# Optimization experiments

Hardware: AMD Instinct MI355X
Metric: run time of the kernel (lower is better)

The kernel has to match this reference:

```python
import jax, jax.numpy as jnp
import numpy as np

B = 256          # batch
MID = 16384      # mid_siz
OUT = 16384      # out_siz
C = 16           # channel_siz
NLVL = 8         # nlvl (== klvl here since floor(log2(OUT/2))=13 >= 8)
MIDF = MID >> NLVL   # mid_filter_siz = 64
OUTF = OUT >> NLVL   # out_filter_siz = 64
NB = 1 << NLVL       # 256 leaf branches
STD = 0.5


def setup_inputs() -> dict:
    key = jax.random.key(0)
    ks = jax.random.split(key, 6)
    in_data = jax.random.normal(ks[0], (B, MID, 2), jnp.float32)
    # learned parameters (buildRand: normal(0, 0.5) filters, zero biases)
    mid_dense = jax.random.normal(ks[1], (1, MID, 2), jnp.float32) * STD
    in_filter = jax.random.normal(ks[2], (MIDF, 1, C), jnp.float32) * STD   # conv1d [width,in,out]
    in_bias = jnp.zeros((C,), jnp.float32)
    # level lvl (1..NLVL) uses filters[lvl-1, :2**lvl]; padded to NB branches
    filters = jax.random.normal(ks[3], (NLVL, NB, 2, C, C), jnp.float32) * STD
    biases = jnp.zeros((NLVL, NB, C), jnp.float32)
    fea_dense = jax.random.normal(ks[4], (NB, C, OUTF), jnp.float32) * STD
    return dict(in_data=in_data, mid_dense=mid_dense, in_filter=in_filter,
                in_bias=in_bias, filters=filters, biases=biases, fea_dense=fea_dense)


def reference(in_data, mid_dense, in_filter, in_bias, filters, biases, fea_dense):
    # elementwise modulation then split real/imag channels: (B, 2, MID)
    x = jnp.moveaxis(in_data * mid_dense, -1, 1)
    # level-0 conv1d: kernel MIDF, stride MIDF//2 -> overlapping half-windows.
    # Split signal into half-width chunks h; window t = [h[t], h[t+1]].
    half = MIDF // 2
    h = x.reshape(B, 2, MID // half, half)                 # (B,2,512,32)
    W1 = in_filter[:half, 0, :]                            # (32,C)
    W2 = in_filter[half:, 0, :]
    s = jnp.einsum('bisw,wc->bisc', h[:, :, :-1], W1) \
        + jnp.einsum('bisw,wc->bisc', h[:, :, 1:], W2)
    s = jax.nn.relu(s + in_bias)                           # (B,2,2^(n+1)-1,C)
    state = s[:, :, None]                                  # (B,2,nb=1,L,C)
    # butterfly tree: each level doubles branches; conv kernel=2, stride=2, VALID
    for lvl in range(1, NLVL + 1):
        nb = 1 << lvl
        p = jnp.repeat(state, 2, axis=2)                   # child itk <- parent itk//2
        L = p.shape[3]                                     # odd: 2^(n+1-lvl+1)-1
        xw = p[:, :, :, :L - 1, :].reshape(B, 2, nb, (L - 1) // 2, 2, C)
        W = filters[lvl - 1, :nb]                          # (nb,2,C,C)
        bb = biases[lvl - 1, :nb]                          # (nb,C)
        state = jax.nn.relu(
            jnp.einsum('bintkc,nkcd->bintd', xw, W) + bb[None, None, :, None, :])
    feat = state[:, :, :, 0, :]                            # (B,2,NB,C): L==1 at last level
    outp = jnp.einsum('binc,ncf->binf', feat, fea_dense)   # per-branch dense projection
    R = outp[:, 0].reshape(B, OUT // 2, 2)
    I = outp[:, 1].reshape(B, OUT // 2, 2)
    out_data = ((R[:, :, 0] - I[:, :, 1]) / MID).reshape(B, OUT // 2, 1)
    return out_data, R[:, :, 1]
```

## Files before the change

kernel.cpp:

```cpp
#include <hip/hip_runtime.h>
#include <hip/hip_bf16.h>


#define OUT_HALF 2097152

typedef __attribute__((ext_vector_type(4))) float f32x4;
typedef __attribute__((ext_vector_type(8))) short s16x8;

__device__ __forceinline__ uint fsw(uint a) {
    return a ^ ((((a >> 6) ^ (a >> 8)) & 3u) << 4);
}
__device__ __forceinline__ ushort bfr(float f) {
    __hip_bfloat16 h = __float2bfloat16(f);
    union { __hip_bfloat16 h; ushort u; } cv; cv.h = h; return cv.u;
}
__device__ __forceinline__ uint pk(float a, float b) {
    return (uint)bfr(a) | ((uint)bfr(b) << 16);
}

__device__ __forceinline__ void tree_level(
    char* smb, const int lane, const int wave,
    uint AOff, uint NOff, int lgR, int lgNP, int nTiles,
    uint WOff, int wnb, uint LBOff, int bnb)
{
    const int m  = lane & 15;
    const int kg = lane >> 4;
    const int lgTPP = lgR - 4;
    for (int at = wave; at < nTiles; at += 4) {
        const int p  = at >> lgTPP;
        const int tc = at & ((1 << lgTPP) - 1);
        const int np = p & ((1 << lgNP) - 1);
        const int ii = p >> lgNP;
        s16x8 af = *(const s16x8*)(smb + AOff + (p << (lgR + 6)) +
                                   fsw((uint)((tc * 16 + m) * 64 + kg * 16)));
#pragma unroll
        for (int sib = 0; sib < 2; sib++) {
            const int nl = 2 * np + sib;
            s16x8 bf = *(const s16x8*)(smb + WOff +
                         fsw((uint)((wnb + nl) * 1024 + m * 64 + kg * 16)));
            float bv = *(const float*)(smb + LBOff + ((bnb + nl) * 16 + m) * 4);
            f32x4 acc = {bv, bv, bv, bv};
            acc = __builtin_amdgcn_mfma_f32_16x16x32_bf16(af, bf, acc, 0, 0, 0);
            const int p2 = (ii << (lgNP + 1)) + nl;
            const uint wb = NOff + (p2 << (lgR + 5));
            const int r2 = tc * 8 + kg * 2;
            *(uint*)(smb + wb + fsw((uint)(r2 * 64 + m * 4))) =
                pk(fmaxf(acc.x, 0.f), fmaxf(acc.y, 0.f));
            *(uint*)(smb + wb + fsw((uint)((r2 + 1) * 64 + m * 4))) =
                pk(fmaxf(acc.z, 0.f), fmaxf(acc.w, 0.f));
        }
    }
}

__global__ __launch_bounds__(256, 4)
void ibf_A(const float* __restrict__ in_data, const float* __restrict__ mid_dense,
           const float* __restrict__ in_filter, const float* __restrict__ in_bias,
           const float* __restrict__ filters, const float* __restrict__ biases,
           uint* __restrict__ S3)
{
    __shared__ __align__(16) char smb[29760];
    const int tid = threadIdx.x, lane = tid & 63, wave = tid >> 6;
    const int b = blockIdx.x;
    const int th = blockIdx.y >> 1;
    const int i  = blockIdx.y & 1;

    {
        const float4* inb = (const float4*)in_data + (size_t)b * 8192 + th * 2048;
        const float4* mdb = (const float4*)mid_dense + th * 2048;
        for (int mp = tid; mp < 2064; mp += 256) {
            float4 iv = inb[mp], mv = mdb[mp];
            float xa = i ? iv.y * mv.y : iv.x * mv.x;
            float xb = i ? iv.w * mv.w : iv.z * mv.z;
            *(uint*)(smb + fsw((uint)(mp * 4))) = pk(xa, xb);
        }
    }
    for (int t = tid; t < 3584; t += 256) {
        int nidx = t >> 8, r = t & 255, d = r & 15, c = r >> 4;
        int lvl = (nidx < 2) ? 1 : ((nidx < 6) ? 2 : 3);
        int n = nidx - ((1 << lvl) - 2);
        const float* src = filters + (size_t)(lvl - 1) * 131072 + n * 512 + c * 16 + d;
        *(uint*)(smb + 12416 + fsw((uint)(nidx * 1024 + d * 64 + c * 4))) = pk(src[0], src[256]);
    }
    for (int t = tid; t < 512; t += 256) {
        int c = t >> 5, w2 = t & 31;
        *(uint*)(smb + 26752 + fsw((uint)(c * 128 + w2 * 4))) =
            pk(in_filter[(2 * w2) * 16 + c], in_filter[(2 * w2 + 1) * 16 + c]);
    }
    if (tid < 240) {
        float v;
        if (tid < 224) {
            int nidx = tid >> 4;
            int lvl = (nidx < 2) ? 1 : ((nidx < 6) ? 2 : 3);
            int n = nidx - ((1 << lvl) - 2);
            v = biases[(size_t)(lvl - 1) * 4096 + n * 16 + (tid & 15)];
        } else v = in_bias[tid - 224];
        *(float*)(smb + 28800 + tid * 4) = v;
    }
    __syncthreads();

    {
        const int m = lane & 15, kg = lane >> 4;
        s16x8 b0 = *(const s16x8*)(smb + 26752 + fsw((uint)(m * 128 + kg * 16)));
        s16x8 b1 = *(const s16x8*)(smb + 26752 + fsw((uint)(m * 128 + 64 + kg * 16)));
        float bv = *(const float*)(smb + 28800 + (224 + m) * 4);
        for (int at = wave; at < 8; at += 4) {
            int tc = at;
            s16x8 a0 = *(const s16x8*)(smb + fsw((uint)((tc * 16 + m) * 64 + kg * 16)));
            s16x8 a1 = *(const s16x8*)(smb + fsw((uint)((tc * 16 + m) * 64 + 64 + kg * 16)));
            f32x4 acc = {bv, bv, bv, bv};
            acc = __builtin_amdgcn_mfma_f32_16x16x32_bf16(a0, b0, acc, 0, 0, 0);
            acc = __builtin_amdgcn_mfma_f32_16x16x32_bf16(a1, b1, acc, 0, 0, 0);
            int r2 = tc * 8 + kg * 2;
            *(uint*)(smb + 8320 + fsw((uint)(r2 * 64 + m * 4))) =
                pk(fmaxf(acc.x, 0.f), fmaxf(acc.y, 0.f));
            *(uint*)(smb + 8320 + fsw((uint)((r2 + 1) * 64 + m * 4))) =
                pk(fmaxf(acc.z, 0.f), fmaxf(acc.w, 0.f));
        }
    }
    __syncthreads();
    tree_level(smb, lane, wave, 8320, 0,    6, 0, 4, 12416, 0, 28800, 0);
    __syncthreads();
    tree_level(smb, lane, wave, 0,    8320, 5, 1, 4, 12416, 2, 28800, 2);
    __syncthreads();
    {
        const int m = lane & 15, kg = lane >> 4;
        for (int at = wave; at < 4; at += 4) {
            s16x8 af = *(const s16x8*)(smb + 8320 + (at << 10) + fsw((uint)(m * 64 + kg * 16)));
#pragma unroll
            for (int sib = 0; sib < 2; sib++) {
                int n3 = 2 * at + sib;
                s16x8 bf = *(const s16x8*)(smb + 12416 +
                             fsw((uint)((6 + n3) * 1024 + m * 64 + kg * 16)));
                float bv = *(const float*)(smb + 28800 + ((6 + n3) * 16 + m) * 4);
                f32x4 acc = {bv, bv, bv, bv};
                acc = __builtin_amdgcn_mfma_f32_16x16x32_bf16(af, bf, acc, 0, 0, 0);
                int bi = 2 * b + i;
                int t4 = th * 8 + kg * 2;
                uint idx = ((uint)(n3 * 512 + bi) * 16 + t4) * 16 + m;
                S3[idx]      = pk(fmaxf(acc.x, 0.f), fmaxf(acc.y, 0.f));
                S3[idx + 16] = pk(fmaxf(acc.z, 0.f), fmaxf(acc.w, 0.f));
            }
        }
    }
}

__global__ __launch_bounds__(256, 2)
void ibf_B(const float* __restrict__ filters, const float* __restrict__ biases,
           const uint* __restrict__ S3, char* __restrict__ S8)
{
    __shared__ __align__(16) char smb[24576];
    const int tid = threadIdx.x, lane = tid & 63, wave = tid >> 6;
    const int n3 = blockIdx.x, chunk = blockIdx.y;
    const int m = lane & 15, kg = lane >> 4;

    const float* FB1 = filters + (size_t)3 * 131072 + ((size_t)(n3 << 1)) * 512;
    const float* FB2 = filters + (size_t)4 * 131072 + ((size_t)(n3 << 2)) * 512;
    const float* FB3 = filters + (size_t)5 * 131072 + ((size_t)(n3 << 3)) * 512;
    const float* FB4 = filters + (size_t)6 * 131072 + ((size_t)(n3 << 4)) * 512;
    const float* FB5 = filters + (size_t)7 * 131072 + ((size_t)(n3 << 5)) * 512;
    const float* BB1 = biases + (size_t)3 * 4096 + (n3 << 1) * 16;
    const float* BB2 = biases + (size_t)4 * 4096 + (n3 << 2) * 16;
    const float* BB3 = biases + (size_t)5 * 4096 + (n3 << 3) * 16;
    const float* BB4 = biases + (size_t)6 * 4096 + (n3 << 4) * 16;
    const float* BB5 = biases + (size_t)7 * 4096 + (n3 << 5) * 16;

#define LDFRAG(dst, fb, nl)                                                  \
    {                                                                        \
        const float* s_ = (fb) + (nl) * 512 + m;                             \
        _Pragma("unroll")                                                    \
        for (int c4 = 0; c4 < 4; c4++) {                                     \
            int c_ = kg * 4 + c4;                                            \
            (&(dst).x)[c4] = pk(s_[c_ * 16], s_[256 + c_ * 16]);             \
        }                                                                    \
    }

    uint4 f4[2], f5[4];
    float b4[2], b5[4];
    LDFRAG(f4[0], FB1, 0); LDFRAG(f4[1], FB1, 1);
    b4[0] = BB1[m]; b4[1] = BB1[16 + m];
#pragma unroll
    for (int s = 0; s < 4; s++) { LDFRAG(f5[s], FB2, s); b5[s] = BB2[s * 16 + m]; }
    {
        const char* src = (const char*)S3 + ((size_t)n3 * 512 + chunk * 8) * 1024;
        for (int ci = tid; ci < 512; ci += 256)
            *(float4*)(smb + fsw((uint)(ci * 16))) = *(const float4*)(src + ci * 16);
    }
    __syncthreads();

    uint4 f6[4];
    float b6[4];
    {
        const int n0 = (wave >> 1) * 2;
        LDFRAG(f6[0], FB3, n0);     b6[0] = BB3[(n0) * 16 + m];
        LDFRAG(f6[1], FB3, n0 + 1); b6[1] = BB3[(n0 + 1) * 16 + m];
        LDFRAG(f6[2], FB3, n0 + 4); b6[2] = BB3[(n0 + 4) * 16 + m];
        LDFRAG(f6[3], FB3, n0 + 5); b6[3] = BB3[(n0 + 5) * 16 + m];
    }
#pragma unroll
    for (int t2 = 0; t2 < 2; t2++) {
        const int tc = wave + t2 * 4;
        s16x8 af = *(const s16x8*)(smb + fsw((uint)((tc * 16 + m) * 64 + kg * 16)));
#pragma unroll
        for (int sib = 0; sib < 2; sib++) {
            f32x4 acc = {b4[sib], b4[sib], b4[sib], b4[sib]};
            acc = __builtin_amdgcn_mfma_f32_16x16x32_bf16(af, *(const s16x8*)&f4[sib], acc, 0, 0, 0);
            const uint wb = 8192u + (uint)sib * 4096u;
            const int r2 = tc * 8 + kg * 2;
            *(uint*)(smb + wb + fsw((uint)(r2 * 64 + m * 4))) = pk(fmaxf(acc.x, 0.f), fmaxf(acc.y, 0.f));
            *(uint*)(smb + wb + fsw((uint)((r2 + 1) * 64 + m * 4))) = pk(fmaxf(acc.z, 0.f), fmaxf(acc.w, 0.f));
        }
    }
    __syncthreads();

    uint4 f7[4];
    float b7[4];
    {
        LDFRAG(f7[0], FB4, 2 * wave);     b7[0] = BB4[(2 * wave) * 16 + m];
        LDFRAG(f7[1], FB4, 2 * wave + 1); b7[1] = BB4[(2 * wave + 1) * 16 + m];
        LDFRAG(f7[2], FB4, 2 * wave + 8); b7[2] = BB4[(2 * wave + 8) * 16 + m];
        LDFRAG(f7[3], FB4, 2 * wave + 9); b7[3] = BB4[(2 * wave + 9) * 16 + m];
    }
#pragma unroll
    for (int t2 = 0; t2 < 2; t2++) {
        const int at = wave + t2 * 4;
        const int p = at >> 2, tc = at & 3;
        s16x8 af = *(const s16x8*)(smb + 8192 + p * 4096 + fsw((uint)((tc * 16 + m) * 64 + kg * 16)));
#pragma unroll
        for (int sib = 0; sib < 2; sib++) {
            const int nl = 2 * p + sib;
            f32x4 acc = {b5[nl], b5[nl], b5[nl], b5[nl]};
            acc = __builtin_amdgcn_mfma_f32_16x16x32_bf16(af, *(const s16x8*)&f5[nl], acc, 0, 0, 0);
            const uint wb = (uint)nl * 2048u;
            const int r2 = tc * 8 + kg * 2;
            *(uint*)(smb + wb + fsw((uint)(r2 * 64 + m * 4))) = pk(fmaxf(acc.x, 0.f), fmaxf(acc.y, 0.f));
            *(uint*)(smb + wb + fsw((uint)((r2 + 1) * 64 + m * 4))) = pk(fmaxf(acc.z, 0.f), fmaxf(acc.w, 0.f));
        }
    }
    __syncthreads();

    uint4 f8[8];
    float b8[8];
#pragma unroll
    for (int t4 = 0; t4 < 4; t4++) {
        const int at = wave + 4 * t4;
        LDFRAG(f8[2 * t4],     FB5, 2 * at);     b8[2 * t4]     = BB5[(2 * at) * 16 + m];
        LDFRAG(f8[2 * t4 + 1], FB5, 2 * at + 1); b8[2 * t4 + 1] = BB5[(2 * at + 1) * 16 + m];
    }
#pragma unroll
    for (int t2 = 0; t2 < 2; t2++) {
        const int at = wave + t2 * 4;
        const int p = at >> 1, tc = at & 1;
        s16x8 af = *(const s16x8*)(smb + p * 2048 + fsw((uint)((tc * 16 + m) * 64 + kg * 16)));
#pragma unroll
        for (int sib = 0; sib < 2; sib++) {
            const int nl = 2 * p + sib;
            const int fi = t2 * 2 + sib;
            f32x4 acc = {b6[fi], b6[fi], b6[fi], b6[fi]};
            acc = __builtin_amdgcn_mfma_f32_16x16x32_bf16(af, *(const s16x8*)&f6[fi], acc, 0, 0, 0);
            const uint wb = 8192u + (uint)nl * 1024u;
            const int r2 = tc * 8 + kg * 2;
            *(uint*)(smb + wb + fsw((uint)(r2 * 64 + m * 4))) = pk(fmaxf(acc.x, 0.f), fmaxf(acc.y, 0.f));
            *(uint*)(smb + wb + fsw((uint)((r2 + 1) * 64 + m * 4))) = pk(fmaxf(acc.z, 0.f), fmaxf(acc.w, 0.f));
        }
    }
    __syncthreads();

#pragma unroll
    for (int t2 = 0; t2 < 2; t2++) {
        const int p = wave + t2 * 4;
        s16x8 af = *(const s16x8*)(smb + 8192 + p * 1024 + fsw((uint)(m * 64 + kg * 16)));
#pragma unroll
        for (int sib = 0; sib < 2; sib++) {
            const int nl = 2 * p + sib;
            const int fi = t2 * 2 + sib;
            f32x4 acc = {b7[fi], b7[fi], b7[fi], b7[fi]};
            acc = __builtin_amdgcn_mfma_f32_16x16x32_bf16(af, *(const s16x8*)&f7[fi], acc, 0, 0, 0);
            const uint wb = (uint)nl * 512u;
            const int r2 = kg * 2;
            *(uint*)(smb + wb + fsw((uint)(r2 * 64 + m * 4))) = pk(fmaxf(acc.x, 0.f), fmaxf(acc.y, 0.f));
            *(uint*)(smb + wb + fsw((uint)((r2 + 1) * 64 + m * 4))) = pk(fmaxf(acc.z, 0.f), fmaxf(acc.w, 0.f));
        }
    }
    __syncthreads();

#pragma unroll
    for (int t4 = 0; t4 < 4; t4++) {
        const int at = wave + 4 * t4;
        s16x8 af = *(const s16x8*)(smb + at * 512 + fsw((uint)(m * 64 + kg * 16)));
#pragma unroll
        for (int sib = 0; sib < 2; sib++) {
            const int nl = 2 * at + sib;
            const int fi = t4 * 2 + sib;
            f32x4 acc = {b8[fi], b8[fi], b8[fi], b8[fi]};
            acc = __builtin_amdgcn_mfma_f32_16x16x32_bf16(af, *(const s16x8*)&f8[fi], acc, 0, 0, 0);
            if (kg < 2) {
                float v[4] = {fmaxf(acc.x, 0.f), fmaxf(acc.y, 0.f),
                              fmaxf(acc.z, 0.f), fmaxf(acc.w, 0.f)};
#pragma unroll
                for (int j = 0; j < 4; j++)
                    *(ushort*)(smb + 16384 + nl * 256 + (kg * 4 + j) * 32 + m * 2) = bfr(v[j]);
            }
        }
    }
    __syncthreads();
    {
        float4* dst = (float4*)(S8 + (size_t)(n3 * 64 + chunk) * 8192);
        for (int ci = tid; ci < 512; ci += 256)
            dst[ci] = *(const float4*)(smb + 16384 + ci * 16);
    }
#undef LDFRAG
}

__global__ __launch_bounds__(256, 4)
void ibf_C(const float* __restrict__ fea_dense, const char* __restrict__ S8,
           float* __restrict__ out)
{
    __shared__ ushort FEb[1024];
    const int tid = threadIdx.x, lane = tid & 63, wave = tid >> 6;
    const int n8g = blockIdx.x, q = blockIdx.y;
    const int n3 = n8g >> 5, n8l = n8g & 31;

    for (int idx = tid; idx < 1024; idx += 256) {
        int c = idx >> 6, u = idx & 63;
        FEb[u * 16 + c] = bfr(fea_dense[(size_t)n8g * 1024 + idx]);
    }
    __syncthreads();

    const int m = lane & 15, kg = lane >> 4;
    s16x8 bfrg[4];
#pragma unroll
    for (int ut = 0; ut < 4; ut++) {
        if (kg < 2) bfrg[ut] = *(const s16x8*)(FEb + (ut * 16 + m) * 16 + kg * 8);
        else        bfrg[ut] = (s16x8){0, 0, 0, 0, 0, 0, 0, 0};
    }
    for (int w = 0; w < 2; w++) {
        const int tile  = q * 8 + wave * 2 + w;
        const int birow = tile * 16 + m;
        s16x8 af = {0, 0, 0, 0, 0, 0, 0, 0};
        if (kg < 2)
            af = *(const s16x8*)(S8 + ((size_t)(n3 * 64 + (birow >> 3)) * 32 + n8l) * 256
                                 + (birow & 7) * 32 + kg * 16);
        const int b0  = (tile * 16 + kg * 4) >> 1;
        const bool odd = (m & 1);
#pragma unroll
        for (int ut = 0; ut < 4; ut++) {
            f32x4 acc = {0.f, 0.f, 0.f, 0.f};
            acc = __builtin_amdgcn_mfma_f32_16x16x32_bf16(af, bfrg[ut], acc, 0, 0, 0);
            float sy = __shfl_xor(acc.y, 1);
            float sw = __shfl_xor(acc.w, 1);
            const int g = n8g * 32 + ut * 8 + (m >> 1);
            float v0 = odd ? acc.x : (acc.x - sy) * (1.f / 16384.f);
            float v1 = odd ? acc.z : (acc.z - sw) * (1.f / 16384.f);
            size_t off = (odd ? (size_t)OUT_HALF : (size_t)0) + (size_t)g;
            out[(size_t)b0 * 8192 + off]       = v0;
            out[(size_t)(b0 + 1) * 8192 + off] = v1;
        }
    }
}

extern "C" void kernel_launch(void* const* d_in, const int* in_sizes, int n_in,
                              void* d_out, int out_size, void* d_ws, size_t ws_size,
                              hipStream_t stream) {
    const float* in_data   = (const float*)d_in[0];
    const float* mid_dense = (const float*)d_in[1];
    const float* in_filter = (const float*)d_in[2];
    const float* in_bias   = (const float*)d_in[3];
    const float* filters   = (const float*)d_in[4];
    const float* biases    = (const float*)d_in[5];
    const float* fea_dense = (const float*)d_in[6];
    float* out = (float*)d_out;
    uint* S3   = (uint*)d_ws;
    char* S8   = (char*)d_ws + (4 << 20);

    ibf_A<<<dim3(256, 4), 256, 0, stream>>>(in_data, mid_dense, in_filter, in_bias,
                                            filters, biases, S3);
    ibf_B<<<dim3(8, 64), 256, 0, stream>>>(filters, biases, S3, S8);
    ibf_C<<<dim3(256, 4), 256, 0, stream>>>(fea_dense, S8, out);
}
```

Measured before the change: 40.55 us.

## Fuse final tree stage with dense projection kernel, eliminating S8 round trip

Merges the last-stage tree kernel and the per-branch dense projection kernel into one kernel. Leaf features stay in shared memory in a swizzled, zero-padded layout and feed the projection MFMA directly, so the S8 workspace write/read and one kernel launch are gone. In exchange, each block now reloads and converts fea_dense from global memory with strided scalar loads, repeated across the 64 chunk blocks. It also raises shared memory per block, and each block does less projection work with fewer lanes active.

```diff
diff --git a/kernel.cpp b/kernel.cpp
--- a/kernel.cpp
+++ b/kernel.cpp
@@ -145,13 +145,17 @@
 }
 
 __global__ __launch_bounds__(256, 2)
-void ibf_B(const float* __restrict__ filters, const float* __restrict__ biases,
-           const uint* __restrict__ S3, char* __restrict__ S8)
+void ibf_BC(const float* __restrict__ filters, const float* __restrict__ biases,
+            const float* __restrict__ fea_dense, const uint* __restrict__ S3,
+            float* __restrict__ out)
 {
-    __shared__ __align__(16) char smb[24576];
+    __shared__ __align__(16) char smb[33536];
     const int tid = threadIdx.x, lane = tid & 63, wave = tid >> 6;
     const int n3 = blockIdx.x, chunk = blockIdx.y;
     const int m = lane & 15, kg = lane >> 4;
+
+    for (int o = tid * 16; o < 16384; o += 4096)
+        *(float4*)(smb + 16384 + o) = make_float4(0.f, 0.f, 0.f, 0.f);
 
     const float* FB1 = filters + (size_t)3 * 131072 + ((size_t)(n3 << 1)) * 512;
     const float* FB2 = filters + (size_t)4 * 131072 + ((size_t)(n3 << 2)) * 512;
@@ -297,65 +301,48 @@
                 float v[4] = {fmaxf(acc.x, 0.f), fmaxf(acc.y, 0.f),
                               fmaxf(acc.z, 0.f), fmaxf(acc.w, 0.f)};
 #pragma unroll
-                for (int j = 0; j < 4; j++)
-                    *(ushort*)(smb + 16384 + nl * 256 + (kg * 4 + j) * 32 + m * 2) = bfr(v[j]);
+                for (int j = 0; j < 4; j++) {
+                    uint o = (uint)(nl * 512 + (kg * 4 + j) * 64 + m * 2);
+                    *(ushort*)(smb + 16384 + fsw(o)) = bfr(v[j]);
+                }
             }
         }
     }
     __syncthreads();
-    {
-        float4* dst = (float4*)(S8 + (size_t)(n3 * 64 + chunk) * 8192);
-        for (int ci = tid; ci < 512; ci += 256)
-            dst[ci] = *(const float4*)(smb + 16384 + ci * 16);
+
+    for (int q = 0; q < 8; q++) {
+        int n8l = wave * 8 + q;
+        int gn8 = n3 * 32 + n8l;
+        s16x8 af = *(const s16x8*)(smb + 16384 +
+                     fsw((uint)(n8l * 512 + m * 64 + kg * 16)));
+        const float* fb = fea_dense + (size_t)gn8 * 1024;
+#pragma unroll
+        for (int ut = 0; ut < 4; ut++) {
+            s16x8 bf = {0, 0, 0, 0, 0, 0, 0, 0};
+            if (kg < 2) {
+                const float* fp = fb + kg * 512 + ut * 16 + m;
+                bf[0] = (short)bfr(fp[0]);   bf[1] = (short)bfr(fp[64]);
+                bf[2] = (short)bfr(fp[128]); bf[3] = (short)bfr(fp[192]);
+                bf[4] = (short)bfr(fp[256]); bf[5] = (short)bfr(fp[320]);
+                bf[6] = (short)bfr(fp[384]); bf[7] = (short)bfr(fp[448]);
+            }
+            f32x4 acc = {0.f, 0.f, 0.f, 0.f};
+            acc = __builtin_amdgcn_mfma_f32_16x16x32_bf16(af, bf, acc, 0, 0, 0);
+            float s0 = __shfl_xor(acc.y, 1);
+            float s2 = __shfl_xor(acc.w, 1);
+            if (kg < 2) {
+                int g = gn8 * 32 + ut * 8 + (m >> 1);
+                bool odd = (m & 1);
+                float v0 = odd ? acc.x : (acc.x - s0) * (1.f / 16384.f);
+                float v1 = odd ? acc.z : (acc.z - s2) * (1.f / 16384.f);
+                size_t off = (odd ? (size_t)OUT_HALF : (size_t)0) + (size_t)g;
+                int b0 = chunk * 4 + kg * 2;
+                out[(size_t)b0 * 8192 + off]       = v0;
+                out[(size_t)(b0 + 1) * 8192 + off] = v1;
+            }
+        }
     }
 #undef LDFRAG
-}
-
-__global__ __launch_bounds__(256, 4)
-void ibf_C(const float* __restrict__ fea_dense, const char* __restrict__ S8,
-           float* __restrict__ out)
-{
-    __shared__ ushort FEb[1024];
-    const int tid = threadIdx.x, lane = tid & 63, wave = tid >> 6;
-    const int n8g = blockIdx.x, q = blockIdx.y;
-    const int n3 = n8g >> 5, n8l = n8g & 31;
-
-    for (int idx = tid; idx < 1024; idx += 256) {
-        int c = idx >> 6, u = idx & 63;
-        FEb[u * 16 + c] = bfr(fea_dense[(size_t)n8g * 1024 + idx]);
-    }
-    __syncthreads();
-
-    const int m = lane & 15, kg = lane >> 4;
-    s16x8 bfrg[4];
-#pragma unroll
-    for (int ut = 0; ut < 4; ut++) {
-        if (kg < 2) bfrg[ut] = *(const s16x8*)(FEb + (ut * 16 + m) * 16 + kg * 8);
-        else        bfrg[ut] = (s16x8){0, 0, 0, 0, 0, 0, 0, 0};
-    }
-    for (int w = 0; w < 2; w++) {
-        const int tile  = q * 8 + wave * 2 + w;
-        const int birow = tile * 16 + m;
-        s16x8 af = {0, 0, 0, 0, 0, 0, 0, 0};
-        if (kg < 2)
-            af = *(const s16x8*)(S8 + ((size_t)(n3 * 64 + (birow >> 3)) * 32 + n8l) * 256
-                                 + (birow & 7) * 32 + kg * 16);
-        const int b0  = (tile * 16 + kg * 4) >> 1;
-        const bool odd = (m & 1);
-#pragma unroll
-        for (int ut = 0; ut < 4; ut++) {
-            f32x4 acc = {0.f, 0.f, 0.f, 0.f};
-            acc = __builtin_amdgcn_mfma_f32_16x16x32_bf16(af, bfrg[ut], acc, 0, 0, 0);
-            float sy = __shfl_xor(acc.y, 1);
-            float sw = __shfl_xor(acc.w, 1);
-            const int g = n8g * 32 + ut * 8 + (m >> 1);
-            float v0 = odd ? acc.x : (acc.x - sy) * (1.f / 16384.f);
-            float v1 = odd ? acc.z : (acc.z - sw) * (1.f / 16384.f);
-            size_t off = (odd ? (size_t)OUT_HALF : (size_t)0) + (size_t)g;
-            out[(size_t)b0 * 8192 + off]       = v0;
-            out[(size_t)(b0 + 1) * 8192 + off] = v1;
-        }
-    }
 }
 
 extern "C" void kernel_launch(void* const* d_in, const int* in_sizes, int n_in,
@@ -370,10 +357,8 @@
     const float* fea_dense = (const float*)d_in[6];
     float* out = (float*)d_out;
     uint* S3   = (uint*)d_ws;
-    char* S8   = (char*)d_ws + (4 << 20);
 
     ibf_A<<<dim3(256, 4), 256, 0, stream>>>(in_data, mid_dense, in_filter, in_bias,
                                             filters, biases, S3);
-    ibf_B<<<dim3(8, 64), 256, 0, stream>>>(filters, biases, S3, S8);
-    ibf_C<<<dim3(256, 4), 256, 0, stream>>>(fea_dense, S8, out);
-}
+    ibf_BC<<<dim3(8, 64), 256, 0, stream>>>(filters, biases, fea_dense, S3, out);
+}
```

Result: no change. 40.70 us (+0.4%).
